# Performance work log

Hardware: AMD Instinct MI355X
Metric: run time of the kernel (lower is better)

## Reference

```python
import jax, jax.numpy as jnp
import numpy as np

DIM = 2048
NUM_HEADS = 16
NUM_KV_HEADS = 4
HEAD_DIM = DIM // NUM_HEADS  # 128
ROPE_BASE = 10000.0
CLIP = 31.0
BLOCK = 128


def fake_quant(w):
    """Blockwise int-ish fake quantization, steady QAT state (ratio=1, clip=31, no noise)."""
    out_f, in_f = w.shape
    pad = (-in_f) % BLOCK
    wp = jnp.pad(w, ((0, 0), (0, pad)))
    wb = wp.reshape(-1, BLOCK)
    # scale computed under no_grad in torch -> stop_gradient
    bmax = jnp.max(jnp.abs(wb), axis=1)
    s = jnp.maximum(bmax / CLIP, 1e-12).astype(jnp.float16)
    s = jnp.maximum(s, jnp.finfo(jnp.float16).tiny).astype(jnp.float32)
    s = jax.lax.stop_gradient(s)[:, None]
    ws = wb / s
    q = ws - jax.lax.stop_gradient(ws) + jax.lax.stop_gradient(
        jnp.round(jnp.clip(ws, -(CLIP + 1.0), CLIP)))  # STE
    qw = (q * s).reshape(out_f, in_f + pad)
    return qw[:, :in_f] if pad > 0 else qw


def rms_norm(x):
    eps = jnp.finfo(x.dtype).eps
    return x * jax.lax.rsqrt(jnp.mean(x * x, axis=-1, keepdims=True) + eps)


def rope_tables(seqlen, dtype):
    inv_freq = 1.0 / (ROPE_BASE ** (jnp.arange(0, HEAD_DIM, 2, dtype=jnp.float32) / HEAD_DIM))
    freqs = jnp.outer(jnp.arange(seqlen, dtype=jnp.float32), inv_freq)  # [S, hd/2]
    return jnp.cos(freqs).astype(dtype), jnp.sin(freqs).astype(dtype)


def apply_rotary(x, cos, sin):
    # x: [B,H,S,hd]; cos/sin: [S,hd/2]
    half = x.shape[-1] // 2
    x1, x2 = x[..., :half], x[..., half:]
    return jnp.concatenate((x1 * cos + x2 * sin, -x1 * sin + x2 * cos), axis=-1)


def setup_inputs() -> dict:
    key = jax.random.key(0)
    ks = jax.random.split(key, 6)
    kv_dim = NUM_KV_HEADS * HEAD_DIM
    std = DIM ** -0.5
    return {
        "x": jax.random.normal(ks[0], (2, 2048, DIM), dtype=jnp.float32),
        "Wq": jax.random.normal(ks[1], (DIM, DIM), dtype=jnp.float32) * std,
        "Wk": jax.random.normal(ks[2], (kv_dim, DIM), dtype=jnp.float32) * std,
        "Wv": jax.random.normal(ks[3], (kv_dim, DIM), dtype=jnp.float32) * std,
        "Wproj": jax.random.normal(ks[4], (DIM, DIM), dtype=jnp.float32) * std,
        "q_gain": jnp.full((NUM_HEADS,), 1.0, dtype=jnp.float32),
    }


def reference(x, Wq, Wk, Wv, Wproj, q_gain):
    B, S, D = x.shape
    H, KV, hd = NUM_HEADS, NUM_KV_HEADS, HEAD_DIM
    q = (x @ fake_quant(Wq).T).reshape(B, S, H, hd).transpose(0, 2, 1, 3)   # [B,H,S,hd]
    k = (x @ fake_quant(Wk).T).reshape(B, S, KV, hd).transpose(0, 2, 1, 3)  # [B,KV,S,hd]
    v = (x @ fake_quant(Wv).T).reshape(B, S, KV, hd).transpose(0, 2, 1, 3)
    q = rms_norm(q)
    k = rms_norm(k)
    cos, sin = rope_tables(S, q.dtype)
    q = apply_rotary(q, cos, sin)
    k = apply_rotary(k, cos, sin)
    q = q * q_gain[None, :, None, None]
    # GQA: expand kv heads
    rep = H // KV
    k = jnp.repeat(k, rep, axis=1)  # [B,H,S,hd]
    v = jnp.repeat(v, rep, axis=1)
    scale = 1.0 / jnp.sqrt(jnp.asarray(hd, dtype=q.dtype))
    scores = jnp.einsum("bhqd,bhkd->bhqk", q, k) * scale
    causal = jnp.tril(jnp.ones((S, S), dtype=bool))
    scores = jnp.where(causal, scores, jnp.asarray(-jnp.inf, dtype=scores.dtype))
    attn = jax.nn.softmax(scores, axis=-1)
    y = jnp.einsum("bhqk,bhkd->bhqd", attn, v)  # [B,H,S,hd]
    y = y.transpose(0, 2, 1, 3).reshape(B, S, D)
    return y @ fake_quant(Wproj).T
```

## Files before the change

### kernel.cpp

```cpp
#include <hip/hip_runtime.h>
#include <hip/hip_bf16.h>
#include <hip/hip_fp16.h>

#define SEQ    2048
#define DMODEL 2048
#define NH     16
#define NKV    4
#define HD     128
#define NTOT   3072
#define MROWS  4096

typedef __attribute__((ext_vector_type(4))) float f32x4;
typedef __attribute__((ext_vector_type(8))) __bf16 bf16x8;
typedef __attribute__((ext_vector_type(8))) unsigned short u16x8;
typedef __attribute__((ext_vector_type(4))) unsigned short u16x4;

__device__ __forceinline__ void async_copy16(const void* g, void* l) {
  __builtin_amdgcn_global_load_lds(
      (const __attribute__((address_space(1))) void*)g,
      (__attribute__((address_space(3))) void*)l, 16, 0, 0);
}

__device__ __forceinline__ unsigned short fto16(float f) {
  __hip_bfloat16 h = __float2bfloat16(f);
  return *(unsigned short*)&h;
}

__device__ __forceinline__ float b2f(unsigned short u) {
  unsigned int t = (unsigned int)u << 16;
  float f;
  __builtin_memcpy(&f, &t, 4);
  return f;
}

__global__ __launch_bounds__(256) void fq_kernel(const float* __restrict__ Wq,
                                                 const float* __restrict__ Wk,
                                                 const float* __restrict__ Wv,
                                                 const float* __restrict__ Wp,
                                                 unsigned short* __restrict__ Wcat,
                                                 unsigned short* __restrict__ Wpq) {
  int g = blockIdx.x * 4 + (threadIdx.x >> 6);
  int lane = threadIdx.x & 63;
  const float* W;
  unsigned short* out;
  int blk;
  if (g < 32768)      { W = Wq; out = Wcat;                          blk = g; }
  else if (g < 40960) { W = Wk; out = Wcat + (size_t)2048 * 2048;    blk = g - 32768; }
  else if (g < 49152) { W = Wv; out = Wcat + (size_t)2560 * 2048;    blk = g - 40960; }
  else                { W = Wp; out = Wpq;                           blk = g - 49152; }
  const float* p = W + (size_t)blk * 128 + lane * 2;
  float w0 = p[0], w1 = p[1];
  float m = fmaxf(fabsf(w0), fabsf(w1));
#pragma unroll
  for (int o = 32; o; o >>= 1) m = fmaxf(m, __shfl_xor(m, o));
  float s = fmaxf(m / 31.0f, 1e-12f);
  s = __half2float(__float2half(s));
  s = fmaxf(s, 6.103515625e-05f);
  float q0 = rintf(fminf(fmaxf(w0 / s, -32.0f), 31.0f)) * s;
  float q1 = rintf(fminf(fmaxf(w1 / s, -32.0f), 31.0f)) * s;
  unsigned short* o16 = out + (size_t)blk * 128 + lane * 2;
  o16[0] = fto16(q0);
  o16[1] = fto16(q1);
}

__global__ __launch_bounds__(256) void conv_kernel(const float* __restrict__ in,
                                                   unsigned short* __restrict__ out,
                                                   int n) {
  int i = (blockIdx.x * blockDim.x + threadIdx.x) * 4;
  if (i >= n) return;
  float4 v = *(const float4*)(in + i);
  ushort4 o;
  o.x = fto16(v.x); o.y = fto16(v.y); o.z = fto16(v.z); o.w = fto16(v.w);
  *(ushort4*)(out + i) = o;
}

#define BM 128
#define BN 128
#define BK 32
template <typename OT>
__global__ __launch_bounds__(256) void gemm_bt(const unsigned short* __restrict__ A,
                                               const unsigned short* __restrict__ Bm,
                                               OT* __restrict__ C,
                                               int M, int N, int K) {
  __shared__ unsigned short As[BM * BK];
  __shared__ unsigned short Bs[BN * BK];
  const int tid = threadIdx.x;
  const int wave = tid >> 6, lane = tid & 63;
  const int quad = lane >> 4, l16 = lane & 15;
  const int m0 = blockIdx.x * BM, n0 = blockIdx.y * BN;
  const int wm = (wave >> 1) * 64, wn = (wave & 1) * 64;
  const int sr = lane >> 2, sc = (lane & 3) * 8;

  const unsigned short* Ag = A + (size_t)m0 * K;
  const unsigned short* Bg = Bm + (size_t)n0 * K;

  f32x4 acc[4][4];
#pragma unroll
  for (int i = 0; i < 4; i++)
#pragma unroll
    for (int j = 0; j < 4; j++) acc[i][j] = f32x4{0.f, 0.f, 0.f, 0.f};

  const int seg0 = wave * 2, seg1 = wave * 2 + 1;
  unsigned short* lA0 = &As[seg0 * 16 * BK];
  unsigned short* lA1 = &As[seg1 * 16 * BK];
  unsigned short* lB0 = &Bs[seg0 * 16 * BK];
  unsigned short* lB1 = &Bs[seg1 * 16 * BK];
  const unsigned short* gA0 = Ag + (size_t)(seg0 * 16 + sr) * K + sc;
  const unsigned short* gA1 = Ag + (size_t)(seg1 * 16 + sr) * K + sc;
  const unsigned short* gB0 = Bg + (size_t)(seg0 * 16 + sr) * K + sc;
  const unsigned short* gB1 = Bg + (size_t)(seg1 * 16 + sr) * K + sc;

  for (int k0 = 0; k0 < K; k0 += BK) {
    __syncthreads();
    async_copy16(gA0 + k0, lA0);
    async_copy16(gA1 + k0, lA1);
    async_copy16(gB0 + k0, lB0);
    async_copy16(gB1 + k0, lB1);
    __syncthreads();
    bf16x8 af[4], bf[4];
#pragma unroll
    for (int t = 0; t < 4; t++)
      af[t] = *(const bf16x8*)&As[(wm + t * 16 + l16) * BK + quad * 8];
#pragma unroll
    for (int t = 0; t < 4; t++)
      bf[t] = *(const bf16x8*)&Bs[(wn + t * 16 + l16) * BK + quad * 8];
#pragma unroll
    for (int i = 0; i < 4; i++)
#pragma unroll
      for (int j = 0; j < 4; j++)
        acc[i][j] = __builtin_amdgcn_mfma_f32_16x16x32_bf16(af[i], bf[j], acc[i][j], 0, 0, 0);
  }
#pragma unroll
  for (int i = 0; i < 4; i++) {
    int row_base = m0 + wm + i * 16 + quad * 4;
#pragma unroll
    for (int j = 0; j < 4; j++) {
      int col = n0 + wn + j * 16 + l16;
#pragma unroll
      for (int r = 0; r < 4; r++) {
        if constexpr (sizeof(OT) == 2)
          C[(size_t)(row_base + r) * N + col] = fto16(acc[i][j][r]);
        else
          C[(size_t)(row_base + r) * N + col] = acc[i][j][r];
      }
    }
  }
}

#define QSCALE 0.12751791437524245f
__global__ __launch_bounds__(256) void normrope_kernel(const unsigned short* __restrict__ qkvb,
                                                       const float* __restrict__ qgain,
                                                       unsigned short* __restrict__ qbuf,
                                                       unsigned short* __restrict__ kbuf) {
  const int i = blockIdx.x;
  const int bz = i >> 11, tok = i & 2047;
  const int wave = threadIdx.x >> 6, lane = threadIdx.x & 63;
  const unsigned short* row = qkvb + (size_t)i * NTOT;

  double invf = pow(10000.0, -(double)(2 * lane) / 128.0);
  float freq = (float)((double)tok * invf);
  float cs = cosf(freq), sn = sinf(freq);

  for (int slot = wave; slot < 20; slot += 4) {
    if (slot < 16) {
      int hh = slot;
      const unsigned short* src = row + hh * HD;
      float x1 = b2f(src[lane]), x2 = b2f(src[lane + 64]);
      float ss = x1 * x1 + x2 * x2;
#pragma unroll
      for (int o = 32; o; o >>= 1) ss += __shfl_xor(ss, o);
      float rn = rsqrtf(ss * (1.0f / 128.0f) + 1.1920929e-07f);
      float n1 = x1 * rn, n2 = x2 * rn;
      float g = qgain[hh] * QSCALE;
      unsigned short* dst = qbuf + ((size_t)(bz * NH + hh) * SEQ + tok) * HD;
      dst[lane]      = fto16((n1 * cs + n2 * sn) * g);
      dst[lane + 64] = fto16((-n1 * sn + n2 * cs) * g);
    } else {
      int hh = slot - 16;
      const unsigned short* src = row + DMODEL + hh * HD;
      float x1 = b2f(src[lane]), x2 = b2f(src[lane + 64]);
      float ss = x1 * x1 + x2 * x2;
#pragma unroll
      for (int o = 32; o; o >>= 1) ss += __shfl_xor(ss, o);
      float rn = rsqrtf(ss * (1.0f / 128.0f) + 1.1920929e-07f);
      float n1 = x1 * rn, n2 = x2 * rn;
      unsigned short* dst = kbuf + ((size_t)(bz * NKV + hh) * SEQ + tok) * HD;
      dst[lane]      = fto16(n1 * cs + n2 * sn);
      dst[lane + 64] = fto16(-n1 * sn + n2 * cs);
    }
  }
}

__global__ __launch_bounds__(256) void vtrans_kernel(const unsigned short* __restrict__ qkvb,
                                                     unsigned short* __restrict__ vtb) {
  __shared__ unsigned short T[64 * 72];
  const int s0 = blockIdx.x * 64;
  const int d0 = blockIdx.y * 64;
  const int bz = blockIdx.z >> 2, h = blockIdx.z & 3;
  const int tid = threadIdx.x;
#pragma unroll
  for (int i = 0; i < 2; ++i) {
    int c = i * 256 + tid;
    int s = c >> 3, ch = c & 7;
    const unsigned short* src =
        qkvb + (size_t)(bz * SEQ + s0 + s) * NTOT + DMODEL + 512 + h * HD + d0 + ch * 8;
    *(u16x8*)&T[s * 72 + ch * 8] = *(const u16x8*)src;
  }
  __syncthreads();
  unsigned short* outg = vtb + (size_t)(bz * NKV + h) * HD * SEQ;
#pragma unroll
  for (int i = 0; i < 2; ++i) {
    int c = i * 256 + tid;
    int d = c >> 3, sc = c & 7;
    u16x8 v;
#pragma unroll
    for (int j = 0; j < 8; ++j) v[j] = T[(sc * 8 + j) * 72 + d];
    *(u16x8*)(outg + (size_t)(d0 + d) * SEQ + s0 + sc * 8) = v;
  }
}

__global__ __launch_bounds__(256, 2) void attn_kernel(const unsigned short* __restrict__ qb,
                                                      const unsigned short* __restrict__ kb,
                                                      const unsigned short* __restrict__ vtb,
                                                      unsigned short* __restrict__ yb) {
  __shared__ unsigned short Ks[64 * 128];
  __shared__ unsigned short Vt[128 * 64];
  __shared__ unsigned short Ps[4][32 * 64];

  const int bx = blockIdx.x;
  const int h = blockIdx.y;
  const int bz = blockIdx.z;
  const int qt = bz ? bx : (15 - bx);
  const int tid = threadIdx.x;
  const int wave = tid >> 6, lane = tid & 63;
  const int quad = lane >> 4, l16 = lane & 15;
  const int q0 = qt * 128;
  const int base0 = q0 + wave * 32;
  const int base1 = base0 + 16;
  const int kdiag0 = base0 >> 6, kdiag1 = base1 >> 6;

  const unsigned short* qg = qb + (size_t)(bz * NH + h) * SEQ * HD;
  const unsigned short* kg = kb + (size_t)(bz * NKV + (h >> 2)) * SEQ * HD;
  const unsigned short* vg = vtb + (size_t)(bz * NKV + (h >> 2)) * HD * SEQ;
  unsigned short* psw = &Ps[wave][0];

  bf16x8 qf[2][4];
#pragma unroll
  for (int sg = 0; sg < 2; ++sg)
#pragma unroll
    for (int ds = 0; ds < 4; ++ds)
      qf[sg][ds] = *(const bf16x8*)(qg + (size_t)(base0 + sg * 16 + l16) * HD + ds * 32 + quad * 8);

  f32x4 oacc[2][8];
#pragma unroll
  for (int sg = 0; sg < 2; ++sg)
#pragma unroll
    for (int j = 0; j < 8; ++j) oacc[sg][j] = f32x4{0.f, 0.f, 0.f, 0.f};
  float m_i[2] = {-__builtin_inff(), -__builtin_inff()};
  float l_i[2] = {0.f, 0.f};

  const int krw = tid >> 4, kgr = tid & 15;
  const int vdw = tid >> 3, vgr = tid & 7;

  const int nkt = 2 * qt + 2;

  u16x8 pk[4], pv[4];
#pragma unroll
  for (int i = 0; i < 4; ++i)
    pk[i] = *(const u16x8*)(kg + (size_t)(i * 16 + krw) * HD + kgr * 8);
#pragma unroll
  for (int i = 0; i < 4; ++i)
    pv[i] = *(const u16x8*)(vg + (size_t)(i * 32 + vdw) * SEQ + vgr * 8);

  for (int kt = 0; kt < nkt; ++kt) {
#pragma unroll
    for (int i = 0; i < 4; ++i) {
      int row = i * 16 + krw;
      *(u16x8*)&Ks[row * 128 + ((kgr ^ (row & 15)) << 3)] = pk[i];
    }
#pragma unroll
    for (int i = 0; i < 4; ++i) {
      int d = i * 32 + vdw;
      *(u16x8*)&Vt[d * 64 + ((vgr ^ (d & 7)) << 3)] = pv[i];
    }
    __syncthreads();

    if (kt + 1 < nkt) {
#pragma unroll
      for (int i = 0; i < 4; ++i)
        pk[i] = *(const u16x8*)(kg + (size_t)((kt + 1) * 64 + i * 16 + krw) * HD + kgr * 8);
#pragma unroll
      for (int i = 0; i < 4; ++i)
        pv[i] = *(const u16x8*)(vg + (size_t)(i * 32 + vdw) * SEQ + (kt + 1) * 64 + vgr * 8);
    }

    const bool act0 = (kt <= kdiag0);
    if (kt <= kdiag1) {
      f32x4 st[2][4];
#pragma unroll
      for (int sg = 0; sg < 2; ++sg)
#pragma unroll
        for (int mt = 0; mt < 4; ++mt) st[sg][mt] = f32x4{0.f, 0.f, 0.f, 0.f};
#pragma unroll
      for (int mt = 0; mt < 4; ++mt)
#pragma unroll
        for (int ds = 0; ds < 4; ++ds) {
          bf16x8 kf = *(const bf16x8*)&Ks[(mt * 16 + l16) * 128 + ((((ds << 2) + quad) ^ l16) << 3)];
          if (act0)
            st[0][mt] = __builtin_amdgcn_mfma_f32_16x16x32_bf16(kf, qf[0][ds], st[0][mt], 0, 0, 0);
          st[1][mt] = __builtin_amdgcn_mfma_f32_16x16x32_bf16(kf, qf[1][ds], st[1][mt], 0, 0, 0);
        }

#pragma unroll
      for (int sg = 0; sg < 2; ++sg) {
        if (sg == 0 && !act0) continue;
        const int base = sg ? base1 : base0;
        const int qrow = base + l16;
        float p[4][4];
        float mx = -__builtin_inff();
        if (kt == (sg ? kdiag1 : kdiag0)) {
#pragma unroll
          for (int mt = 0; mt < 4; ++mt)
#pragma unroll
            for (int r = 0; r < 4; ++r) {
              int kp = kt * 64 + mt * 16 + quad * 4 + r;
              float v = (kp <= qrow) ? st[sg][mt][r] : -__builtin_inff();
              p[mt][r] = v;
              mx = fmaxf(mx, v);
            }
        } else {
#pragma unroll
          for (int mt = 0; mt < 4; ++mt)
#pragma unroll
            for (int r = 0; r < 4; ++r) {
              p[mt][r] = st[sg][mt][r];
              mx = fmaxf(mx, st[sg][mt][r]);
            }
        }
        mx = fmaxf(mx, __shfl_xor(mx, 16));
        mx = fmaxf(mx, __shfl_xor(mx, 32));
        float mnew = fmaxf(m_i[sg], mx);
        float rs = 0.f;
#pragma unroll
        for (int mt = 0; mt < 4; ++mt)
#pragma unroll
          for (int r = 0; r < 4; ++r) {
            float e = exp2f(p[mt][r] - mnew);
            p[mt][r] = e;
            rs += e;
          }
        rs += __shfl_xor(rs, 16);
        rs += __shfl_xor(rs, 32);
        if (__any(mnew > m_i[sg])) {
          float a = exp2f(m_i[sg] - mnew);
#pragma unroll
          for (int j = 0; j < 8; ++j) oacc[sg][j] *= a;
          l_i[sg] = l_i[sg] * a + rs;
        } else {
          l_i[sg] += rs;
        }
        m_i[sg] = mnew;

        const int rq = sg * 16 + l16;
#pragma unroll
        for (int mt = 0; mt < 4; ++mt) {
          u16x4 w;
#pragma unroll
          for (int r = 0; r < 4; ++r) w[r] = fto16(p[mt][r]);
          int g = mt * 2 + (quad >> 1);
          *(u16x4*)&psw[rq * 64 + ((g ^ (l16 & 7)) << 3) + (quad & 1) * 4] = w;
        }
      }

      __asm__ volatile("s_waitcnt lgkmcnt(0)" ::: "memory");

#pragma unroll
      for (int c = 0; c < 2; ++c) {
        bf16x8 pf0, pf1;
        if (act0)
          pf0 = *(const bf16x8*)&psw[l16 * 64 + ((((c << 2) + quad) ^ (l16 & 7)) << 3)];
        pf1 = *(const bf16x8*)&psw[(16 + l16) * 64 + ((((c << 2) + quad) ^ (l16 & 7)) << 3)];
#pragma unroll
        for (int mt = 0; mt < 8; ++mt) {
          bf16x8 vf = *(const bf16x8*)&Vt[(mt * 16 + l16) * 64 + ((((c << 2) + quad) ^ (l16 & 7)) << 3)];
          if (act0)
            oacc[0][mt] = __builtin_amdgcn_mfma_f32_16x16x32_bf16(vf, pf0, oacc[0][mt], 0, 0, 0);
          oacc[1][mt] = __builtin_amdgcn_mfma_f32_16x16x32_bf16(vf, pf1, oacc[1][mt], 0, 0, 0);
        }
      }
    }
    __syncthreads();
  }

#pragma unroll
  for (int sg = 0; sg < 2; ++sg) {
    float il = 1.0f / l_i[sg];
    int qrow = base0 + sg * 16 + l16;
#pragma unroll
    for (int mt = 0; mt < 8; ++mt) {
      u16x4 o;
#pragma unroll
      for (int r = 0; r < 4; ++r) o[r] = fto16(oacc[sg][mt][r] * il);
      *(u16x4*)&yb[(size_t)(bz * SEQ + qrow) * DMODEL + h * HD + mt * 16 + quad * 4] = o;
    }
  }
}

extern "C" void kernel_launch(void* const* d_in, const int* in_sizes, int n_in,
                              void* d_out, int out_size, void* d_ws, size_t ws_size,
                              hipStream_t stream) {
  (void)in_sizes; (void)n_in; (void)out_size; (void)ws_size;
  const float* x  = (const float*)d_in[0];
  const float* Wq = (const float*)d_in[1];
  const float* Wk = (const float*)d_in[2];
  const float* Wv = (const float*)d_in[3];
  const float* Wp = (const float*)d_in[4];
  const float* qg = (const float*)d_in[5];
  float* out = (float*)d_out;
  char* ws = (char*)d_ws;

  unsigned short* xb   = (unsigned short*)(ws + 0);
  unsigned short* Wcat = (unsigned short*)(ws + 16777216);
  unsigned short* Wpq  = (unsigned short*)(ws + 29360128);
  unsigned short* qkvb = (unsigned short*)(ws + 37748736);
  unsigned short* qbuf = (unsigned short*)(ws + 62914560);
  unsigned short* kbuf = (unsigned short*)(ws + 79691776);
  unsigned short* vtb  = (unsigned short*)(ws + 83886080);
  unsigned short* yb   = xb;

  fq_kernel<<<81920 / 4, 256, 0, stream>>>(Wq, Wk, Wv, Wp, Wcat, Wpq);
  conv_kernel<<<8388608 / 1024, 256, 0, stream>>>(x, xb, 8388608);
  gemm_bt<unsigned short><<<dim3(32, 24), 256, 0, stream>>>(xb, Wcat, qkvb, MROWS, NTOT, DMODEL);
  normrope_kernel<<<MROWS, 256, 0, stream>>>(qkvb, qg, qbuf, kbuf);
  vtrans_kernel<<<dim3(32, 2, 8), 256, 0, stream>>>(qkvb, vtb);
  attn_kernel<<<dim3(16, NH, 2), 256, 0, stream>>>(qbuf, kbuf, vtb, yb);
  gemm_bt<float><<<dim3(32, 16), 256, 0, stream>>>(yb, Wpq, out, MROWS, DMODEL, DMODEL);
}
```

Baseline: 336.3 us.

## Double-buffer attention K/V, keep P in registers with fp16 MFMA, swizzle GEMM LDS

The attention kernel now double-buffers K and V tiles in shared memory, so the next tile is written during the current compute and one barrier per iteration is removed. The probability tile no longer goes through LDS: it is converted to fp16 in registers and fed straight into 16x16x16 f16 MFMAs, with V transposed into fp16 to match. The GEMM uses an XOR-swizzled LDS layout to reduce bank conflicts, and RoPE uses fast float sincos and exp2 in place of double pow. In exchange the kernel uses more LDS, fp16 P and V change precision, and the fast sincos is less accurate at large angles.

```diff
diff --git a/kernel.cpp b/kernel.cpp
--- a/kernel.cpp
+++ b/kernel.cpp
@@ -12,6 +12,7 @@
 
 typedef __attribute__((ext_vector_type(4))) float f32x4;
 typedef __attribute__((ext_vector_type(8))) __bf16 bf16x8;
+typedef __attribute__((ext_vector_type(4))) _Float16 f16x4;
 typedef __attribute__((ext_vector_type(8))) unsigned short u16x8;
 typedef __attribute__((ext_vector_type(4))) unsigned short u16x4;
 
@@ -89,7 +90,6 @@
   const int quad = lane >> 4, l16 = lane & 15;
   const int m0 = blockIdx.x * BM, n0 = blockIdx.y * BN;
   const int wm = (wave >> 1) * 64, wn = (wave & 1) * 64;
-  const int sr = lane >> 2, sc = (lane & 3) * 8;
 
   const unsigned short* Ag = A + (size_t)m0 * K;
   const unsigned short* Bg = Bm + (size_t)n0 * K;
@@ -100,15 +100,21 @@
 #pragma unroll
     for (int j = 0; j < 4; j++) acc[i][j] = f32x4{0.f, 0.f, 0.f, 0.f};
 
-  const int seg0 = wave * 2, seg1 = wave * 2 + 1;
-  unsigned short* lA0 = &As[seg0 * 16 * BK];
-  unsigned short* lA1 = &As[seg1 * 16 * BK];
-  unsigned short* lB0 = &Bs[seg0 * 16 * BK];
-  unsigned short* lB1 = &Bs[seg1 * 16 * BK];
-  const unsigned short* gA0 = Ag + (size_t)(seg0 * 16 + sr) * K + sc;
-  const unsigned short* gA1 = Ag + (size_t)(seg1 * 16 + sr) * K + sc;
-  const unsigned short* gB0 = Bg + (size_t)(seg0 * 16 + sr) * K + sc;
-  const unsigned short* gB1 = Bg + (size_t)(seg1 * 16 + sr) * K + sc;
+  const int rp  = lane >> 3;
+  const int ggs = (lane & 7) ^ rp;
+  const int sro = rp * 2 + (ggs >> 2);
+  const int sco = (ggs & 3) * 8;
+  const int seg0 = wave * 2, seg1 = seg0 + 1;
+  unsigned short* lA0 = &As[seg0 * 512];
+  unsigned short* lA1 = &As[seg1 * 512];
+  unsigned short* lB0 = &Bs[seg0 * 512];
+  unsigned short* lB1 = &Bs[seg1 * 512];
+  const unsigned short* gA0 = Ag + (size_t)(seg0 * 16 + sro) * K + sco;
+  const unsigned short* gA1 = Ag + (size_t)(seg1 * 16 + sro) * K + sco;
+  const unsigned short* gB0 = Bg + (size_t)(seg0 * 16 + sro) * K + sco;
+  const unsigned short* gB1 = Bg + (size_t)(seg1 * 16 + sro) * K + sco;
+
+  const int fbase = (l16 >> 1) * 64 + ((((((l16 & 1) << 2) | quad)) ^ ((l16 >> 1) & 7)) << 3);
 
   for (int k0 = 0; k0 < K; k0 += BK) {
     __syncthreads();
@@ -120,10 +126,10 @@
     bf16x8 af[4], bf[4];
 #pragma unroll
     for (int t = 0; t < 4; t++)
-      af[t] = *(const bf16x8*)&As[(wm + t * 16 + l16) * BK + quad * 8];
+      af[t] = *(const bf16x8*)&As[(wm + t * 16) * 32 + fbase];
 #pragma unroll
     for (int t = 0; t < 4; t++)
-      bf[t] = *(const bf16x8*)&Bs[(wn + t * 16 + l16) * BK + quad * 8];
+      bf[t] = *(const bf16x8*)&Bs[(wn + t * 16) * 32 + fbase];
 #pragma unroll
     for (int i = 0; i < 4; i++)
 #pragma unroll
@@ -157,9 +163,10 @@
   const int wave = threadIdx.x >> 6, lane = threadIdx.x & 63;
   const unsigned short* row = qkvb + (size_t)i * NTOT;
 
-  double invf = pow(10000.0, -(double)(2 * lane) / 128.0);
-  float freq = (float)((double)tok * invf);
-  float cs = cosf(freq), sn = sinf(freq);
+  float invf = exp2f(-0.10381025296f * (float)(2 * lane));
+  float freq = (float)tok * invf;
+  float cs, sn;
+  __sincosf(freq, &sn, &cs);
 
   for (int slot = wave; slot < 20; slot += 4) {
     if (slot < 16) {
@@ -204,7 +211,16 @@
     int s = c >> 3, ch = c & 7;
     const unsigned short* src =
         qkvb + (size_t)(bz * SEQ + s0 + s) * NTOT + DMODEL + 512 + h * HD + d0 + ch * 8;
-    *(u16x8*)&T[s * 72 + ch * 8] = *(const u16x8*)src;
+    u16x8 sv = *(const u16x8*)src;
+    u16x8 v;
+#pragma unroll
+    for (int j = 0; j < 8; ++j) {
+      __half hf = __float2half(b2f(sv[j]));
+      unsigned short b;
+      __builtin_memcpy(&b, &hf, 2);
+      v[j] = b;
+    }
+    *(u16x8*)&T[s * 72 + ch * 8] = v;
   }
   __syncthreads();
   unsigned short* outg = vtb + (size_t)(bz * NKV + h) * HD * SEQ;
@@ -223,9 +239,8 @@
                                                       const unsigned short* __restrict__ kb,
                                                       const unsigned short* __restrict__ vtb,
                                                       unsigned short* __restrict__ yb) {
-  __shared__ unsigned short Ks[64 * 128];
-  __shared__ unsigned short Vt[128 * 64];
-  __shared__ unsigned short Ps[4][32 * 64];
+  __shared__ unsigned short Ks[2][64 * 128];
+  __shared__ unsigned short Vt[2][128 * 64];
 
   const int bx = blockIdx.x;
   const int h = blockIdx.y;
@@ -236,13 +251,11 @@
   const int quad = lane >> 4, l16 = lane & 15;
   const int q0 = qt * 128;
   const int base0 = q0 + wave * 32;
-  const int base1 = base0 + 16;
-  const int kdiag0 = base0 >> 6, kdiag1 = base1 >> 6;
+  const int kdiag0 = base0 >> 6, kdiag1 = (base0 + 16) >> 6;
 
   const unsigned short* qg = qb + (size_t)(bz * NH + h) * SEQ * HD;
   const unsigned short* kg = kb + (size_t)(bz * NKV + (h >> 2)) * SEQ * HD;
   const unsigned short* vg = vtb + (size_t)(bz * NKV + (h >> 2)) * HD * SEQ;
-  unsigned short* psw = &Ps[wave][0];
 
   bf16x8 qf[2][4];
 #pragma unroll
@@ -261,7 +274,6 @@
 
   const int krw = tid >> 4, kgr = tid & 15;
   const int vdw = tid >> 3, vgr = tid & 7;
-
   const int nkt = 2 * qt + 2;
 
   u16x8 pk[4], pv[4];
@@ -271,21 +283,25 @@
 #pragma unroll
   for (int i = 0; i < 4; ++i)
     pv[i] = *(const u16x8*)(vg + (size_t)(i * 32 + vdw) * SEQ + vgr * 8);
+#pragma unroll
+  for (int i = 0; i < 4; ++i) {
+    int row = i * 16 + krw;
+    *(u16x8*)&Ks[0][row * 128 + ((kgr ^ (row & 15)) << 3)] = pk[i];
+  }
+#pragma unroll
+  for (int i = 0; i < 4; ++i) {
+    int d = i * 32 + vdw;
+    *(u16x8*)&Vt[0][d * 64 + ((vgr ^ (d & 7)) << 3)] = pv[i];
+  }
+  __syncthreads();
 
   for (int kt = 0; kt < nkt; ++kt) {
-#pragma unroll
-    for (int i = 0; i < 4; ++i) {
-      int row = i * 16 + krw;
-      *(u16x8*)&Ks[row * 128 + ((kgr ^ (row & 15)) << 3)] = pk[i];
-    }
-#pragma unroll
-    for (int i = 0; i < 4; ++i) {
-      int d = i * 32 + vdw;
-      *(u16x8*)&Vt[d * 64 + ((vgr ^ (d & 7)) << 3)] = pv[i];
-    }
-    __syncthreads();
-
-    if (kt + 1 < nkt) {
+    const int cur = kt & 1;
+    const unsigned short* KsC = &Ks[cur][0];
+    const unsigned short* VtC = &Vt[cur][0];
+    const bool pre = (kt + 1 < nkt);
+
+    if (pre) {
 #pragma unroll
       for (int i = 0; i < 4; ++i)
         pk[i] = *(const u16x8*)(kg + (size_t)((kt + 1) * 64 + i * 16 + krw) * HD + kgr * 8);
@@ -305,17 +321,17 @@
       for (int mt = 0; mt < 4; ++mt)
 #pragma unroll
         for (int ds = 0; ds < 4; ++ds) {
-          bf16x8 kf = *(const bf16x8*)&Ks[(mt * 16 + l16) * 128 + ((((ds << 2) + quad) ^ l16) << 3)];
+          bf16x8 kf = *(const bf16x8*)&KsC[(mt * 16 + l16) * 128 + ((((ds << 2) + quad) ^ l16) << 3)];
           if (act0)
             st[0][mt] = __builtin_amdgcn_mfma_f32_16x16x32_bf16(kf, qf[0][ds], st[0][mt], 0, 0, 0);
           st[1][mt] = __builtin_amdgcn_mfma_f32_16x16x32_bf16(kf, qf[1][ds], st[1][mt], 0, 0, 0);
         }
 
+      f16x4 bp[2][4];
 #pragma unroll
       for (int sg = 0; sg < 2; ++sg) {
         if (sg == 0 && !act0) continue;
-        const int base = sg ? base1 : base0;
-        const int qrow = base + l16;
+        const int qrow = base0 + sg * 16 + l16;
         float p[4][4];
         float mx = -__builtin_inff();
         if (kt == (sg ? kdiag1 : kdiag0)) {
@@ -360,33 +376,39 @@
           l_i[sg] += rs;
         }
         m_i[sg] = mnew;
-
-        const int rq = sg * 16 + l16;
 #pragma unroll
         for (int mt = 0; mt < 4; ++mt) {
-          u16x4 w;
-#pragma unroll
-          for (int r = 0; r < 4; ++r) w[r] = fto16(p[mt][r]);
-          int g = mt * 2 + (quad >> 1);
-          *(u16x4*)&psw[rq * 64 + ((g ^ (l16 & 7)) << 3) + (quad & 1) * 4] = w;
+          f16x4 w;
+#pragma unroll
+          for (int r = 0; r < 4; ++r) w[r] = (_Float16)p[mt][r];
+          bp[sg][mt] = w;
         }
       }
 
-      __asm__ volatile("s_waitcnt lgkmcnt(0)" ::: "memory");
-
-#pragma unroll
-      for (int c = 0; c < 2; ++c) {
-        bf16x8 pf0, pf1;
-        if (act0)
-          pf0 = *(const bf16x8*)&psw[l16 * 64 + ((((c << 2) + quad) ^ (l16 & 7)) << 3)];
-        pf1 = *(const bf16x8*)&psw[(16 + l16) * 64 + ((((c << 2) + quad) ^ (l16 & 7)) << 3)];
-#pragma unroll
-        for (int mt = 0; mt < 8; ++mt) {
-          bf16x8 vf = *(const bf16x8*)&Vt[(mt * 16 + l16) * 64 + ((((c << 2) + quad) ^ (l16 & 7)) << 3)];
+#pragma unroll
+      for (int mt = 0; mt < 4; ++mt) {
+        const int g = 2 * mt + (quad >> 1);
+        const int vo = ((g ^ (l16 & 7)) << 3) + (quad & 1) * 4;
+#pragma unroll
+        for (int dt = 0; dt < 8; ++dt) {
+          f16x4 vf = *(const f16x4*)&VtC[(dt * 16 + l16) * 64 + vo];
           if (act0)
-            oacc[0][mt] = __builtin_amdgcn_mfma_f32_16x16x32_bf16(vf, pf0, oacc[0][mt], 0, 0, 0);
-          oacc[1][mt] = __builtin_amdgcn_mfma_f32_16x16x32_bf16(vf, pf1, oacc[1][mt], 0, 0, 0);
+            oacc[0][dt] = __builtin_amdgcn_mfma_f32_16x16x16f16(vf, bp[0][mt], oacc[0][dt], 0, 0, 0);
+          oacc[1][dt] = __builtin_amdgcn_mfma_f32_16x16x16f16(vf, bp[1][mt], oacc[1][dt], 0, 0, 0);
         }
+      }
+    }
+
+    if (pre) {
+#pragma unroll
+      for (int i = 0; i < 4; ++i) {
+        int row = i * 16 + krw;
+        *(u16x8*)&Ks[cur ^ 1][row * 128 + ((kgr ^ (row & 15)) << 3)] = pk[i];
+      }
+#pragma unroll
+      for (int i = 0; i < 4; ++i) {
+        int d = i * 32 + vdw;
+        *(u16x8*)&Vt[cur ^ 1][d * 64 + ((vgr ^ (d & 7)) << 3)] = pv[i];
       }
     }
     __syncthreads();
@@ -397,11 +419,11 @@
     float il = 1.0f / l_i[sg];
     int qrow = base0 + sg * 16 + l16;
 #pragma unroll
-    for (int mt = 0; mt < 8; ++mt) {
+    for (int dt = 0; dt < 8; ++dt) {
       u16x4 o;
 #pragma unroll
-      for (int r = 0; r < 4; ++r) o[r] = fto16(oacc[sg][mt][r] * il);
-      *(u16x4*)&yb[(size_t)(bz * SEQ + qrow) * DMODEL + h * HD + mt * 16 + quad * 4] = o;
+      for (int r = 0; r < 4; ++r) o[r] = fto16(oacc[sg][dt][r] * il);
+      *(u16x4*)&yb[(size_t)(bz * SEQ + qrow) * DMODEL + h * HD + dt * 16 + quad * 4] = o;
     }
   }
 }
```

Result: slower. 349.9 us (+4.1%).
